# Performance work log

Hardware: AMD Instinct MI355X
Metric: run time of the kernel (lower is better)

## Reference

```python
import jax, jax.numpy as jnp
import numpy as np

NUM_BINS = 10


def setup_inputs() -> dict:
    key = jax.random.key(0)
    k1, k2 = jax.random.split(key)
    resmap = jax.random.uniform(k1, (64, 512, 512), dtype=jnp.float32)  # scores in [0,1)
    gtmap = jax.random.uniform(k2, (64, 1, 512, 512), dtype=jnp.float32)  # soft gt mask
    return {"resmap": resmap, "gtmap": gtmap}


def reference(resmap, gtmap):
    # Flatten everything: the loop nest iterates over all b*n elements.
    res = resmap.reshape(-1)
    gt = gtmap.reshape(-1)
    # Bin index = int(res / 0.1): truncation toward zero; clip for safety at res==1.0.
    bins = jnp.clip((res / 0.1).astype(jnp.int32), 0, NUM_BINS - 1)
    ano = gt > 0.5
    ano_count = jax.ops.segment_sum(ano.astype(jnp.int32), bins, num_segments=NUM_BINS)
    nor_count = jax.ops.segment_sum((~ano).astype(jnp.int32), bins, num_segments=NUM_BINS)
    return ano_count, nor_count
```

## Files before the change

### kernel.cpp

```cpp
#include <hip/hip_runtime.h>

#define NUM_BINS 10
#define GRID1 2048
#define BLOCK 256

typedef float f32x4 __attribute__((ext_vector_type(4)));

__device__ __forceinline__ void accum_quad(f32x4 r, f32x4 g, int p[5]) {
    #pragma unroll
    for (int j = 0; j < 4; ++j) {
        float rv = r[j];
        float gv = g[j];
        int b = (int)(rv * 10.0f);
        b = b > NUM_BINS - 1 ? NUM_BINS - 1 : b;
        int c = (gv > 0.5f) ? b : b + NUM_BINS;
        int inc = 1 << ((c & 3) << 3);
        int sel = c >> 2;
        #pragma unroll
        for (int k = 0; k < 5; ++k)
            p[k] += (sel == k) ? inc : 0;
    }
}

__global__ __launch_bounds__(BLOCK) void hist_asm(
    const float* __restrict__ res,
    const float* __restrict__ gt,
    int* __restrict__ out,
    int n4)
{
    const int tid  = threadIdx.x;
    const int lane = tid & 63;
    const int wv   = tid >> 6;

    int p[5] = {0, 0, 0, 0, 0};

    const f32x4* __restrict__ res4 = (const f32x4*)res;
    const f32x4* __restrict__ gt4  = (const f32x4*)gt;

    const int S    = GRID1 * BLOCK;
    const int base = blockIdx.x * BLOCK + tid;

    if (n4 == S * 8) {
        const f32x4* rp = res4 + base;
        const f32x4* gp = gt4 + base;
        f32x4 r[8], g[8];
        #pragma unroll
        for (int k = 0; k < 8; ++k) {
            asm volatile("global_load_dwordx4 %0, %1, off"
                         : "=&v"(r[k]) : "v"(rp + (size_t)k * S));
            asm volatile("global_load_dwordx4 %0, %1, off"
                         : "=&v"(g[k]) : "v"(gp + (size_t)k * S));
        }
        __builtin_amdgcn_sched_barrier(0);
        asm volatile("s_waitcnt vmcnt(0)" ::: "memory");
        __builtin_amdgcn_sched_barrier(0);
        #pragma unroll
        for (int k = 0; k < 8; ++k)
            accum_quad(r[k], g[k], p);
    } else {
        for (int i = base; i < n4; i += S)
            accum_quad(res4[i], gt4[i], p);
    }

    #pragma unroll
    for (int k = 0; k < 5; ++k) {
        p[k] += __shfl_xor(p[k], 1, 64);
        p[k] += __shfl_xor(p[k], 2, 64);
    }
    int q[10];
    #pragma unroll
    for (int k = 0; k < 5; ++k) {
        q[2 * k]     = p[k] & 0x00FF00FF;
        q[2 * k + 1] = (p[k] >> 8) & 0x00FF00FF;
    }
    #pragma unroll
    for (int m = 4; m <= 32; m <<= 1) {
        #pragma unroll
        for (int k = 0; k < 10; ++k)
            q[k] += __shfl_xor(q[k], m, 64);
    }

    __shared__ int part[4][2 * NUM_BINS];
    if (lane == 0) {
        #pragma unroll
        for (int k = 0; k < 5; ++k) {
            part[wv][4 * k + 0] = q[2 * k] & 0xFFFF;
            part[wv][4 * k + 2] = (int)((unsigned)q[2 * k] >> 16);
            part[wv][4 * k + 1] = q[2 * k + 1] & 0xFFFF;
            part[wv][4 * k + 3] = (int)((unsigned)q[2 * k + 1] >> 16);
        }
    }
    __syncthreads();
    if (tid < 2 * NUM_BINS) {
        int s = part[0][tid] + part[1][tid] + part[2][tid] + part[3][tid];
        if (s) atomicAdd(&out[tid], s);
    }
}

extern "C" void kernel_launch(void* const* d_in, const int* in_sizes, int n_in,
                              void* d_out, int out_size, void* d_ws, size_t ws_size,
                              hipStream_t stream) {
    const float* res = (const float*)d_in[0];
    const float* gt  = (const float*)d_in[1];
    int* out = (int*)d_out;

    const int n  = in_sizes[0];
    const int n4 = n >> 2;

    hipMemsetAsync(d_out, 0, 2 * NUM_BINS * sizeof(int), stream);
    hist_asm<<<GRID1, BLOCK, 0, stream>>>(res, gt, out, n4);
}
```

Measured before the change: 45.56 us.

## Stream inputs through LDS via global_load_lds DMA in serialized chunks

Replaces the register-staged batch of 16 dwordx4 global loads per thread with direct global-to-LDS loads (global_load_lds, 16 bytes per lane) into 2048-float shared buffers. Each block now processes a contiguous slice in four chunks, with a barrier before and after each chunk's loads. The aim is to cut VGPR pressure and issue overhead. In exchange, each chunk's memory latency is exposed and not overlapped, since there is no double buffering, and there are extra barriers and LDS reads.

```diff
diff --git a/kernel.cpp b/kernel.cpp
--- a/kernel.cpp
+++ b/kernel.cpp
@@ -3,8 +3,17 @@
 #define NUM_BINS 10
 #define GRID1 2048
 #define BLOCK 256
+#define CHUNK 2048
+#define ITERS 4
+#define EPB (CHUNK * ITERS)
 
 typedef float f32x4 __attribute__((ext_vector_type(4)));
+
+__device__ __forceinline__ void gld_lds16(const float* g, float* l) {
+    __builtin_amdgcn_global_load_lds(
+        (const __attribute__((address_space(1))) void*)g,
+        (__attribute__((address_space(3))) void*)l, 16, 0, 0);
+}
 
 __device__ __forceinline__ void accum_quad(f32x4 r, f32x4 g, int p[5]) {
     #pragma unroll
@@ -22,43 +31,46 @@
     }
 }
 
-__global__ __launch_bounds__(BLOCK) void hist_asm(
+__global__ __launch_bounds__(BLOCK) void hist_ldsdma(
     const float* __restrict__ res,
     const float* __restrict__ gt,
     int* __restrict__ out,
-    int n4)
+    int n)
 {
+    __shared__ float sres[CHUNK];
+    __shared__ float sgt[CHUNK];
+
     const int tid  = threadIdx.x;
     const int lane = tid & 63;
     const int wv   = tid >> 6;
 
     int p[5] = {0, 0, 0, 0, 0};
 
-    const f32x4* __restrict__ res4 = (const f32x4*)res;
-    const f32x4* __restrict__ gt4  = (const f32x4*)gt;
-
-    const int S    = GRID1 * BLOCK;
-    const int base = blockIdx.x * BLOCK + tid;
-
-    if (n4 == S * 8) {
-        const f32x4* rp = res4 + base;
-        const f32x4* gp = gt4 + base;
-        f32x4 r[8], g[8];
+    if (n == GRID1 * EPB) {
+        const size_t eb = (size_t)blockIdx.x * EPB;
         #pragma unroll
-        for (int k = 0; k < 8; ++k) {
-            asm volatile("global_load_dwordx4 %0, %1, off"
-                         : "=&v"(r[k]) : "v"(rp + (size_t)k * S));
-            asm volatile("global_load_dwordx4 %0, %1, off"
-                         : "=&v"(g[k]) : "v"(gp + (size_t)k * S));
+        for (int it = 0; it < ITERS; ++it) {
+            const float* sr = res + eb + (size_t)it * CHUNK;
+            const float* sg = gt  + eb + (size_t)it * CHUNK;
+            __syncthreads();
+            gld_lds16(sr + tid * 4,        &sres[tid * 4]);
+            gld_lds16(sr + 1024 + tid * 4, &sres[1024 + tid * 4]);
+            gld_lds16(sg + tid * 4,        &sgt[tid * 4]);
+            gld_lds16(sg + 1024 + tid * 4, &sgt[1024 + tid * 4]);
+            __syncthreads();
+            f32x4 r0 = *(const f32x4*)&sres[tid * 8];
+            f32x4 r1 = *(const f32x4*)&sres[tid * 8 + 4];
+            f32x4 g0 = *(const f32x4*)&sgt[tid * 8];
+            f32x4 g1 = *(const f32x4*)&sgt[tid * 8 + 4];
+            accum_quad(r0, g0, p);
+            accum_quad(r1, g1, p);
         }
-        __builtin_amdgcn_sched_barrier(0);
-        asm volatile("s_waitcnt vmcnt(0)" ::: "memory");
-        __builtin_amdgcn_sched_barrier(0);
-        #pragma unroll
-        for (int k = 0; k < 8; ++k)
-            accum_quad(r[k], g[k], p);
     } else {
-        for (int i = base; i < n4; i += S)
+        const f32x4* res4 = (const f32x4*)res;
+        const f32x4* gt4  = (const f32x4*)gt;
+        const int n4 = n >> 2;
+        const int S  = GRID1 * BLOCK;
+        for (int i = blockIdx.x * BLOCK + tid; i < n4; i += S)
             accum_quad(res4[i], gt4[i], p);
     }
 
@@ -104,9 +116,8 @@
     const float* gt  = (const float*)d_in[1];
     int* out = (int*)d_out;
 
-    const int n  = in_sizes[0];
-    const int n4 = n >> 2;
+    const int n = in_sizes[0];
 
     hipMemsetAsync(d_out, 0, 2 * NUM_BINS * sizeof(int), stream);
-    hist_asm<<<GRID1, BLOCK, 0, stream>>>(res, gt, out, n4);
+    hist_ldsdma<<<GRID1, BLOCK, 0, stream>>>(res, gt, out, n);
 }
```

After: 48.17 us. 5.7% more time.
